# Kernel tuning notes

Hardware: AMD Instinct MI355X
Metric: run time of the kernel (lower is better)

The kernel has to match this reference:

```python
import jax, jax.numpy as jnp
import numpy as np

B, N, NUM_CLASS = 32, 4096, 40


def setup_inputs() -> dict:
    key = jax.random.key(0)
    ks = jax.random.split(key, 16)
    def w(k, o, i):
        return (jax.random.normal(k, (o, i), jnp.float32) / np.float32(np.sqrt(i)))
    inp = {"x": jax.random.uniform(ks[0], (B, N, 3), jnp.float32)}
    dims = [("sa1", 3, [64, 64, 128]), ("sa2", 3 + 128, [128, 128, 256]), ("sa3", 3 + 256, [256, 512, 1024])]
    ki = 1
    for name, cin, hs in dims:
        c = cin
        for j, h in enumerate(hs):
            inp[f"{name}_w{j}"] = w(jax.random.fold_in(ks[ki], j), h, c)
            inp[f"{name}_b{j}"] = jnp.zeros((h,), jnp.float32)
            c = h
        ki += 1
    for name, o, i in [("fc1", 512, 1024), ("fc2", 256, 512), ("fc3", NUM_CLASS, 256)]:
        inp[f"{name}_w"] = w(ks[ki], o, i)
        inp[f"{name}_b"] = jnp.zeros((o,), jnp.float32)
        ki += 1
    return inp


def _fps(xyz, npoint):
    # farthest point sampling for a single cloud, xyz: [N, 3] -> [npoint] indices
    n = xyz.shape[0]
    def body(carry, _):
        mind, last = carry
        d = jnp.sum((xyz - xyz[last]) ** 2, axis=-1)
        mind = jnp.minimum(mind, d)
        return (mind, jnp.argmax(mind).astype(jnp.int32)), last
    init = (jnp.full((n,), 1e10, xyz.dtype), jnp.int32(0))
    _, idx = jax.lax.scan(body, init, None, length=npoint)
    return idx


def _ball_query(new_xyz, xyz, radius, nsample):
    # new_xyz: [B,S,3], xyz: [B,N,3] -> [B,S,nsample] neighbor indices
    n = xyz.shape[1]
    sqd = (jnp.sum(new_xyz ** 2, -1)[:, :, None]
           + jnp.sum(xyz ** 2, -1)[:, None, :]
           - 2.0 * jnp.einsum('bsc,bnc->bsn', new_xyz, xyz))  # [B,S,N]
    gid = jnp.where(sqd <= radius ** 2, jnp.arange(n, dtype=jnp.int32), jnp.int32(n))
    gid = jnp.sort(gid, axis=-1)[..., :nsample]
    first = gid[..., :1]
    return jnp.where(gid == n, first, gid)


def _gather(x, idx):
    # x: [B,N,C], idx: [B,S,K] -> [B,S,K,C]
    return jax.vmap(lambda xb, ib: xb[ib])(x, idx)


def _shared_mlp(feat, layers):
    # feat: [..., C_in]; layers: list of (W [C_out,C_in], b [C_out]); 1x1 conv + ReLU (BN folded)
    for W, b in layers:
        feat = jax.nn.relu(jnp.einsum('bskc,oc->bsko', feat, W) + b)
    return feat


def _set_abstraction(xyz, feat, npoint, radius, nsample, layers):
    fidx = jax.vmap(lambda p: _fps(p, npoint))(xyz)            # [B,S]
    new_xyz = jax.vmap(lambda p, i: p[i])(xyz, fidx)           # [B,S,3]
    idx = _ball_query(new_xyz, xyz, radius, nsample)           # [B,S,K]
    gxyz = _gather(xyz, idx) - new_xyz[:, :, None, :]          # relative coords
    g = gxyz if feat is None else jnp.concatenate([gxyz, _gather(feat, idx)], axis=-1)
    g = _shared_mlp(g, layers)
    return new_xyz, jnp.max(g, axis=2)                         # max-pool over ball


def _sa_group_all(xyz, feat, layers):
    g = jnp.concatenate([xyz, feat], axis=-1)[:, None]         # [B,1,N,3+C]
    g = _shared_mlp(g, layers)
    return jnp.max(g, axis=2)[:, 0]                            # [B, 1024]


def reference(x,
              sa1_w0, sa1_b0, sa1_w1, sa1_b1, sa1_w2, sa1_b2,
              sa2_w0, sa2_b0, sa2_w1, sa2_b1, sa2_w2, sa2_b2,
              sa3_w0, sa3_b0, sa3_w1, sa3_b1, sa3_w2, sa3_b2,
              fc1_w, fc1_b, fc2_w, fc2_b, fc3_w, fc3_b):
    xyz, feat = x, None
    xyz, feat = _set_abstraction(xyz, feat, 512, 0.2, 32,
                                 [(sa1_w0, sa1_b0), (sa1_w1, sa1_b1), (sa1_w2, sa1_b2)])
    xyz, feat = _set_abstraction(xyz, feat, 128, 0.4, 64,
                                 [(sa2_w0, sa2_b0), (sa2_w1, sa2_b1), (sa2_w2, sa2_b2)])
    feat = _sa_group_all(xyz, feat,
                         [(sa3_w0, sa3_b0), (sa3_w1, sa3_b1), (sa3_w2, sa3_b2)])
    h = jax.nn.relu(feat @ fc1_w.T + fc1_b)
    h = jax.nn.relu(h @ fc2_w.T + fc2_b)
    logits = h @ fc3_w.T + fc3_b
    return jax.nn.softmax(logits, axis=-1)  # eval-mode output
```

## Files before the change

### kernel.cpp

```cpp
#include <hip/hip_runtime.h>
#include <math.h>

#define B_ 32
#define N_ 4096

typedef __attribute__((ext_vector_type(8))) short short8;
typedef __attribute__((ext_vector_type(4))) float f32x4;
typedef __attribute__((ext_vector_type(2))) float v2f;
typedef __attribute__((ext_vector_type(2))) unsigned u32x2;
typedef __attribute__((ext_vector_type(2))) unsigned long long u64x2;

__device__ __forceinline__ unsigned short f2bf(float f) {
    unsigned u = __float_as_uint(f);
    unsigned r = 0x7FFFu + ((u >> 16) & 1u);
    return (unsigned short)((u + r) >> 16);
}
__device__ __forceinline__ float bf2f(unsigned short h) {
    return __uint_as_float(((unsigned)h) << 16);
}
__device__ __forceinline__ void f2bfpair(float v, short& h, short& l) {
    unsigned short hh = f2bf(v);
    h = (short)hh;
    l = (short)f2bf(v - bf2f(hh));
}

#define KEY_BIAS 0x3F800000u

__device__ __forceinline__ double mk_key(unsigned hi, unsigned lo) {
    u32x2 p;
    p[0] = lo;
    p[1] = hi;
    return __builtin_bit_cast(double, p);
}

__device__ __forceinline__ unsigned long long u64max(unsigned long long a,
                                                     unsigned long long b) {
    return a > b ? a : b;
}
template<int CTRL>
__device__ __forceinline__ double dpp_dbl(double k) {
    unsigned long long u = (unsigned long long)__double_as_longlong(k);
    int lo = __builtin_amdgcn_mov_dpp((int)(unsigned)u, CTRL, 0xf, 0xf, true);
    int hi = __builtin_amdgcn_mov_dpp((int)(unsigned)(u >> 32), CTRL, 0xf, 0xf, true);
    unsigned long long r = ((unsigned long long)(unsigned)hi << 32) | (unsigned)lo;
    return __longlong_as_double((long long)r);
}
__device__ __forceinline__ double wave_argmax_dbl_leader(double key) {
    key = fmax(key, dpp_dbl<0x128>(key));
    key = fmax(key, dpp_dbl<0x124>(key));
    key = fmax(key, dpp_dbl<0x122>(key));
    key = fmax(key, dpp_dbl<0x121>(key));
    key = fmax(key, dpp_dbl<0x142>(key));
    key = fmax(key, dpp_dbl<0x143>(key));
    return key;
}

struct WDesc { const float* src; short* dh; short* dl; int R, C, Cp, blk0, perm; };
struct WDescs { WDesc d[8]; float* gfeat; int gblk0, gtotal; };

__device__ __forceinline__ void wprep_body(const WDescs& W, int blk, int tid) {
    if (blk >= W.gblk0) {
        const int i = (blk - W.gblk0) * 256 + tid;
        if (i < W.gtotal) W.gfeat[i] = 0.f;
        return;
    }
    int di = 0;
#pragma unroll
    for (int k = 1; k < 8; k++) di = (blk >= W.d[k].blk0) ? k : di;
    const WDesc D = W.d[di];
    const int i = (blk - D.blk0) * 256 + tid;
    if (i >= D.R * D.Cp) return;
    const int r = i / D.Cp, c = i % D.Cp;
    int cs;
    if (D.perm) cs = (c < 128) ? c + 3 : (c < 131 ? c - 128 : -1);
    else        cs = (c < D.C) ? c : -1;
    float v = (cs >= 0) ? D.src[r * D.C + cs] : 0.f;
    short h, l;
    f2bfpair(v, h, l);
    D.dh[i] = h; D.dl[i] = l;
}

template<int N, int NPOINT, int NT, int FPSB>
__global__ __launch_bounds__(NT, 1) void fps_wprep_kernel(
    const float* __restrict__ xyz, float* __restrict__ outXyz, WDescs W) {
#pragma clang fp contract(off)
    const int t = threadIdx.x;
    if (blockIdx.x >= FPSB) {
        wprep_body(W, blockIdx.x - FPSB, t);
        return;
    }
    const int b = blockIdx.x;
    constexpr int PPT = N / NT;
    constexpr int PP2 = PPT / 2;
    constexpr int NW = (NT + 63) / 64;
    __shared__ float ps[N][4];
    __shared__ __align__(16) double red[2][NW];
    __shared__ float outBuf[NPOINT * 3];
    const float* base = xyz + (size_t)b * N * 3;
    for (int j = t; j < N; j += NT) {
        ps[j][0] = base[j * 3 + 0];
        ps[j][1] = base[j * 3 + 1];
        ps[j][2] = base[j * 3 + 2];
    }
    __syncthreads();
    v2f px2[PP2], py2[PP2], pz2[PP2], mn2[PP2];
    unsigned nA[PP2], nB[PP2];
#pragma unroll
    for (int j = 0; j < PP2; j++) {
        const int p0 = t + (2 * j) * NT;
        const int p1 = t + (2 * j + 1) * NT;
        f32x4 a = *(const f32x4*)&ps[p0][0];
        f32x4 c = *(const f32x4*)&ps[p1][0];
        px2[j] = (v2f){a[0], c[0]};
        py2[j] = (v2f){a[1], c[1]};
        pz2[j] = (v2f){a[2], c[2]};
        mn2[j] = (v2f){1e10f, 1e10f};
        nA[j] = ~(unsigned)p0;
        nB[j] = ~(unsigned)p1;
    }
#pragma unroll
    for (int j = 0; j < PP2; j++)
        asm volatile("" : "+v"(px2[j]), "+v"(py2[j]), "+v"(pz2[j]));
    float lx = ps[0][0], ly = ps[0][1], lz = ps[0][2];
    if (t == 0) {
        outBuf[0] = lx; outBuf[1] = ly; outBuf[2] = lz;
    }
    for (int it = 1; it < NPOINT; it++) {
        const v2f lx2 = (v2f){lx, lx};
        const v2f ly2 = (v2f){ly, ly};
        const v2f lz2 = (v2f){lz, lz};
        double k0 = 0.0, k1 = 0.0, k2 = 0.0, k3 = 0.0;
#pragma unroll
        for (int j = 0; j < PP2; j++) {
            v2f dx = px2[j] - lx2;
            v2f dy = py2[j] - ly2;
            v2f dz = pz2[j] - lz2;
            v2f t0 = dx * dx, t1 = dy * dy, t2 = dz * dz;
            v2f d2 = (t0 + t1) + t2;
            v2f m = __builtin_elementwise_min(mn2[j], d2);
            mn2[j] = m;
            double da = mk_key(__float_as_uint(m[0]) + KEY_BIAS, nA[j]);
            double db = mk_key(__float_as_uint(m[1]) + KEY_BIAS, nB[j]);
            if (j & 1) { k2 = fmax(k2, da); k3 = fmax(k3, db); }
            else       { k0 = fmax(k0, da); k1 = fmax(k1, db); }
        }
        double key = fmax(fmax(k0, k1), fmax(k2, k3));
        key = wave_argmax_dbl_leader(key);
        const int par = it & 1;
        if ((t & 63) == 63) red[par][t >> 6] = key;
        __syncthreads();
        u64x2 r01 = *(const u64x2*)&red[par][0];
        u64x2 r23 = *(const u64x2*)&red[par][2];
        double b0 = __longlong_as_double((long long)r01[0]);
        double b1 = __longlong_as_double((long long)r01[1]);
        double b2 = __longlong_as_double((long long)r23[0]);
        double b3 = __longlong_as_double((long long)r23[1]);
        double best = fmax(fmax(b0, b1), fmax(b2, b3));
        const int fi = (int)(~(unsigned)(unsigned long long)__double_as_longlong(best));
        f32x4 c4 = *(const f32x4*)&ps[fi][0];
        lx = c4[0]; ly = c4[1]; lz = c4[2];
        if (t == 0) {
            outBuf[it * 3 + 0] = lx;
            outBuf[it * 3 + 1] = ly;
            outBuf[it * 3 + 2] = lz;
        }
    }
    __syncthreads();
    float* dst = outXyz + (size_t)b * NPOINT * 3;
    for (int j = t; j < NPOINT * 3; j += NT) dst[j] = outBuf[j];
}

template<int N, int NS>
__device__ __forceinline__ void ballquery_body(
    const float* __restrict__ xyz, const float* __restrict__ newXyz,
    int* __restrict__ outIdx, int S, float r2, int qid, int lane) {
#pragma clang fp contract(off)
    const int b = qid / S;
    const float* q = newXyz + (size_t)qid * 3;
    const float qx = q[0], qy = q[1], qz = q[2];
    const float qn = (qx * qx + qy * qy) + qz * qz;
    const float* base = xyz + (size_t)b * N * 3;
    int* dst = outIdx + (size_t)qid * NS;
    int cnt = 0, first = 0;
    for (int p0 = 0; p0 < N; p0 += 64) {
        const int p = p0 + lane;
        const float x = base[p * 3 + 0];
        const float y = base[p * 3 + 1];
        const float z = base[p * 3 + 2];
        const float pn = (x * x + y * y) + z * z;
        const float dot = (qx * x + qy * y) + qz * z;
        const float sqd = (qn + pn) - 2.0f * dot;
        const unsigned long long mask = __ballot(sqd <= r2);
        if (mask) {
            if (cnt == 0) first = p0 + __ffsll((unsigned long long)mask) - 1;
            const int prefix = __builtin_amdgcn_mbcnt_hi(
                (unsigned)(mask >> 32),
                __builtin_amdgcn_mbcnt_lo((unsigned)mask, 0));
            const bool in = (mask >> lane) & 1ull;
            const int pos = cnt + prefix;
            if (in && pos < NS) dst[pos] = p;
            cnt += __popcll(mask);
            if (cnt >= NS) break;
        }
    }
    for (int i = cnt + lane; i < NS; i += 64) dst[i] = first;
}

template<int FPB, int BQB, int NQ, int NS, int SQ, int NF, int NPF>
__global__ __launch_bounds__(256) void bq_fps_kernel(
    const float* __restrict__ xyzQ, const float* __restrict__ newXyzQ,
    int* __restrict__ outIdxQ, float r2,
    const float* __restrict__ xyzF, float* __restrict__ outXyzF) {
#pragma clang fp contract(off)
    const int t = threadIdx.x;
    const int lane = t & 63, wv = t >> 6;
    __shared__ float ps[NF][4];
    if (blockIdx.x >= FPB) {
        ballquery_body<NQ, NS>(xyzQ, newXyzQ, outIdxQ, SQ, r2,
                               (blockIdx.x - FPB) * 4 + wv, lane);
        return;
    }
    const int b = blockIdx.x;
    const float* base = xyzF + (size_t)b * NF * 3;
    for (int j = t; j < NF; j += 256) {
        ps[j][0] = base[j * 3 + 0];
        ps[j][1] = base[j * 3 + 1];
        ps[j][2] = base[j * 3 + 2];
    }
    __syncthreads();
    if (t >= 64) return;
    constexpr int PPT = NF / 64;
    constexpr int PP2 = PPT / 2;
    v2f px2[PP2], py2[PP2], pz2[PP2], mn2[PP2];
    unsigned nA[PP2], nB[PP2];
#pragma unroll
    for (int j = 0; j < PP2; j++) {
        const int p0 = t + (2 * j) * 64;
        const int p1 = t + (2 * j + 1) * 64;
        f32x4 a = *(const f32x4*)&ps[p0][0];
        f32x4 c = *(const f32x4*)&ps[p1][0];
        px2[j] = (v2f){a[0], c[0]};
        py2[j] = (v2f){a[1], c[1]};
        pz2[j] = (v2f){a[2], c[2]};
        mn2[j] = (v2f){1e10f, 1e10f};
        nA[j] = ~(unsigned)p0;
        nB[j] = ~(unsigned)p1;
    }
    float lx = ps[0][0], ly = ps[0][1], lz = ps[0][2];
    if (t == 0) {
        outXyzF[(size_t)b * NPF * 3 + 0] = lx;
        outXyzF[(size_t)b * NPF * 3 + 1] = ly;
        outXyzF[(size_t)b * NPF * 3 + 2] = lz;
    }
    for (int it = 1; it < NPF; it++) {
        const v2f lx2 = (v2f){lx, lx};
        const v2f ly2 = (v2f){ly, ly};
        const v2f lz2 = (v2f){lz, lz};
        double k0 = 0.0, k1 = 0.0;
#pragma unroll
        for (int j = 0; j < PP2; j++) {
            v2f dx = px2[j] - lx2;
            v2f dy = py2[j] - ly2;
            v2f dz = pz2[j] - lz2;
            v2f t0 = dx * dx, t1 = dy * dy, t2 = dz * dz;
            v2f d2 = (t0 + t1) + t2;
            v2f m = __builtin_elementwise_min(mn2[j], d2);
            mn2[j] = m;
            double da = mk_key(__float_as_uint(m[0]) + KEY_BIAS, nA[j]);
            double db = mk_key(__float_as_uint(m[1]) + KEY_BIAS, nB[j]);
            k0 = fmax(k0, da);
            k1 = fmax(k1, db);
        }
        double key = fmax(k0, k1);
        key = wave_argmax_dbl_leader(key);
        const int lo = __shfl(
            (int)(unsigned)(unsigned long long)__double_as_longlong(key), 63);
        const int fi = (int)(~(unsigned)lo);
        f32x4 c4 = *(const f32x4*)&ps[fi][0];
        lx = c4[0]; ly = c4[1]; lz = c4[2];
        if (t == 0) {
            outXyzF[((size_t)b * NPF + it) * 3 + 0] = lx;
            outXyzF[((size_t)b * NPF + it) * 3 + 1] = ly;
            outXyzF[((size_t)b * NPF + it) * 3 + 2] = lz;
        }
    }
}

template<int NT, int KS>
__device__ __forceinline__ void mfma_layer(
    const short* Aph, const short* Apl, const int sA,
    const short* __restrict__ Wph, const short* __restrict__ Wpl, const int sW,
    f32x4* acc, const int n0, const int mh, const int lr, const int lq) {
#pragma unroll
    for (int ks = 0; ks < KS; ks++) {
        const int ka = ks * 32 + lq * 8;
        short8 a_h[2], a_l[2];
#pragma unroll
        for (int mt = 0; mt < 2; mt++) {
            const int m = (mh * 2 + mt) * 16 + lr;
            a_h[mt] = *(const short8*)(Aph + m * sA + ka);
            a_l[mt] = *(const short8*)(Apl + m * sA + ka);
        }
#pragma unroll
        for (int nt = 0; nt < NT; nt++) {
            const int n = n0 + nt * 16 + lr;
            short8 b_h = *(const short8*)(Wph + (size_t)n * sW + ka);
            short8 b_l = *(const short8*)(Wpl + (size_t)n * sW + ka);
#pragma unroll
            for (int mt = 0; mt < 2; mt++) {
                f32x4 c = acc[mt * NT + nt];
                c = __builtin_amdgcn_mfma_f32_16x16x32_bf16(a_h[mt], b_h, c, 0, 0, 0);
                c = __builtin_amdgcn_mfma_f32_16x16x32_bf16(a_h[mt], b_l, c, 0, 0, 0);
                c = __builtin_amdgcn_mfma_f32_16x16x32_bf16(a_l[mt], b_h, c, 0, 0, 0);
                acc[mt * NT + nt] = c;
            }
        }
    }
}

template<int NT>
__device__ __forceinline__ void init_bias(f32x4* acc, const float* __restrict__ bias,
                                          const int n0, const int lr) {
#pragma unroll
    for (int nt = 0; nt < NT; nt++) {
        float bv = bias[n0 + nt * 16 + lr];
        f32x4 c = {bv, bv, bv, bv};
        acc[0 * NT + nt] = c;
        acc[1 * NT + nt] = c;
    }
}

template<int NT>
__device__ __forceinline__ void store_split(
    const f32x4* acc, short* Hp, short* Lp, const int stride,
    const int n0, const int mh, const int lr, const int lq) {
#pragma unroll
    for (int mt = 0; mt < 2; mt++)
#pragma unroll
        for (int nt = 0; nt < NT; nt++)
#pragma unroll
            for (int r = 0; r < 4; r++) {
                float v = fmaxf(acc[mt * NT + nt][r], 0.f);
                short h, l;
                f2bfpair(v, h, l);
                const int m = (mh * 2 + mt) * 16 + lq * 4 + r;
                const int n = n0 + nt * 16 + lr;
                Hp[m * stride + n] = h;
                Lp[m * stride + n] = l;
            }
}

#define T1 72
template<int BQ2B>
__global__ __launch_bounds__(256) void sa1_bq2_kernel(
    const float* __restrict__ x, const float* __restrict__ nxyz1,
    const int* __restrict__ idx,
    const float* __restrict__ w0, const float* __restrict__ b0,
    const short* __restrict__ w1h, const short* __restrict__ w1l,
    const float* __restrict__ b1,
    const short* __restrict__ w2h, const short* __restrict__ w2l,
    const float* __restrict__ b2,
    short* __restrict__ feat1h, short* __restrict__ feat1l,
    const float* __restrict__ nxyz2, int* __restrict__ idx2, float r2q) {
    const int t = threadIdx.x;
    const int lane = t & 63, wv = t >> 6;
    if (blockIdx.x < BQ2B) {
        ballquery_body<512, 64>(nxyz1, nxyz2, idx2, 128, r2q,
                                blockIdx.x * 4 + wv, lane);
        return;
    }
    const int g0 = (blockIdx.x - BQ2B) * 2;
    const int b = g0 >> 9;
    const int lr = lane & 15, lq = lane >> 4;
    const int mh = wv & 1, nh = wv >> 1;
    __shared__ float gx[64][4];
    __shared__ short H1h[64 * T1], H1l[64 * T1];
    __shared__ short H2h[64 * T1], H2l[64 * T1];
    if (t < 64) {
        int g = g0 + (t >> 5);
        int id = idx[(size_t)g * 32 + (t & 31)];
        const float* pp = x + ((size_t)b * N_ + id) * 3;
        const float* cc = nxyz1 + (size_t)g * 3;
        gx[t][0] = pp[0] - cc[0];
        gx[t][1] = pp[1] - cc[1];
        gx[t][2] = pp[2] - cc[2];
    }
    __syncthreads();
    {
        const int m = t >> 2, oc = (t & 3) * 16;
        float a0 = gx[m][0], a1 = gx[m][1], a2 = gx[m][2];
        short8 hv0, hv1, lv0, lv1;
#pragma unroll
        for (int i = 0; i < 16; i++) {
            int o = oc + i;
            float v = fmaf(w0[o * 3 + 0], a0,
                      fmaf(w0[o * 3 + 1], a1,
                      fmaf(w0[o * 3 + 2], a2, b0[o])));
            v = fmaxf(v, 0.f);
            short h, l;
            f2bfpair(v, h, l);
            if (i < 8) { hv0[i] = h; lv0[i] = l; }
            else       { hv1[i - 8] = h; lv1[i - 8] = l; }
        }
        *(short8*)&H1h[m * T1 + oc]     = hv0;
        *(short8*)&H1h[m * T1 + oc + 8] = hv1;
        *(short8*)&H1l[m * T1 + oc]     = lv0;
        *(short8*)&H1l[m * T1 + oc + 8] = lv1;
    }
    __syncthreads();
    {
        f32x4 acc[4];
        init_bias<2>(acc, b1, nh * 32, lr);
        mfma_layer<2, 2>(H1h, H1l, T1, w1h, w1l, 64, acc, nh * 32, mh, lr, lq);
        store_split<2>(acc, H2h, H2l, T1, nh * 32, mh, lr, lq);
    }
    __syncthreads();
    {
        f32x4 acc[8];
        init_bias<4>(acc, b2, nh * 64, lr);
        mfma_layer<4, 2>(H2h, H2l, T1, w2h, w2l, 64, acc, nh * 64, mh, lr, lq);
#pragma unroll
        for (int nt = 0; nt < 4; nt++) {
            float v = 0.f;
#pragma unroll
            for (int mt = 0; mt < 2; mt++)
#pragma unroll
                for (int r = 0; r < 4; r++)
                    v = fmaxf(v, acc[mt * 4 + nt][r]);
            v = fmaxf(v, __shfl_xor(v, 16));
            v = fmaxf(v, __shfl_xor(v, 32));
            if (lane < 16) {
                short h, l;
                f2bfpair(v, h, l);
                size_t o = (size_t)(g0 + mh) * 128 + nh * 64 + nt * 16 + lane;
                feat1h[o] = h;
                feat1l[o] = l;
            }
        }
    }
}

#define S1 168
#define S2 136
__global__ __launch_bounds__(256) void sa2_mfma_kernel(
    const float* __restrict__ xyz1,
    const short* __restrict__ feat1h, const short* __restrict__ feat1l,
    const float* __restrict__ newXyz, const int* __restrict__ idx,
    const short* __restrict__ w0h, const short* __restrict__ w0l,
    const float* __restrict__ b0,
    const short* __restrict__ w1h, const short* __restrict__ w1l,
    const float* __restrict__ b1,
    const short* __restrict__ w2h, const short* __restrict__ w2l,
    const float* __restrict__ b2,
    short* __restrict__ a3h, short* __restrict__ a3l) {
    const int g = blockIdx.x;
    const int b = g >> 7;
    const int t = threadIdx.x;
    const int lane = t & 63, wv = t >> 6;
    const int lr = lane & 15, lq = lane >> 4;
    const int mh = wv & 1, nh = wv >> 1;
    __shared__ short Ah[64 * S1], Al[64 * S1];
    __shared__ short Hh[64 * S2], Hl[64 * S2];
    __shared__ float pmax[2][256];
    __shared__ int ids[64];
    if (t < 64) ids[t] = idx[(size_t)g * 64 + t];
    __syncthreads();
    {
        const int m = t >> 2, q = t & 3;
        const int id = ids[m];
        const size_t frow = ((size_t)b * 512 + id) * 128;
#pragma unroll
        for (int c8 = 0; c8 < 4; c8++) {
            const int k = q * 32 + c8 * 8;
            *(short8*)&Ah[m * S1 + k] = *(const short8*)(feat1h + frow + k);
            *(short8*)&Al[m * S1 + k] = *(const short8*)(feat1l + frow + k);
        }
        if (t < 64) {
            const int id2 = ids[t];
            short8 zz = {0, 0, 0, 0, 0, 0, 0, 0};
            *(short8*)&Ah[t * S1 + 128] = zz;
            *(short8*)&Ah[t * S1 + 136] = zz;
            *(short8*)&Ah[t * S1 + 144] = zz;
            *(short8*)&Ah[t * S1 + 152] = zz;
            *(short8*)&Al[t * S1 + 128] = zz;
            *(short8*)&Al[t * S1 + 136] = zz;
            *(short8*)&Al[t * S1 + 144] = zz;
            *(short8*)&Al[t * S1 + 152] = zz;
            const float* prow = xyz1 + ((size_t)b * 512 + id2) * 3;
            const float* crow = newXyz + (size_t)g * 3;
#pragma unroll
            for (int c = 0; c < 3; c++) {
                short h, l;
                f2bfpair(prow[c] - crow[c], h, l);
                Ah[t * S1 + 128 + c] = h;
                Al[t * S1 + 128 + c] = l;
            }
        }
    }
    __syncthreads();
    {
        f32x4 acc[8];
        init_bias<4>(acc, b0, nh * 64, lr);
        mfma_layer<4, 5>(Ah, Al, S1, w0h, w0l, 160, acc, nh * 64, mh, lr, lq);
        store_split<4>(acc, Hh, Hl, S2, nh * 64, mh, lr, lq);
    }
    __syncthreads();
    {
        f32x4 acc[8];
        init_bias<4>(acc, b1, nh * 64, lr);
        mfma_layer<4, 4>(Hh, Hl, S2, w1h, w1l, 128, acc, nh * 64, mh, lr, lq);
        store_split<4>(acc, Ah, Al, S2, nh * 64, mh, lr, lq);
    }
    __syncthreads();
    {
        f32x4 acc[16];
        init_bias<8>(acc, b2, nh * 128, lr);
        mfma_layer<8, 4>(Ah, Al, S2, w2h, w2l, 128, acc, nh * 128, mh, lr, lq);
#pragma unroll
        for (int nt = 0; nt < 8; nt++) {
            float v = 0.f;
#pragma unroll
            for (int mt = 0; mt < 2; mt++)
#pragma unroll
                for (int r = 0; r < 4; r++)
                    v = fmaxf(v, acc[mt * 8 + nt][r]);
            v = fmaxf(v, __shfl_xor(v, 16));
            v = fmaxf(v, __shfl_xor(v, 32));
            if (lane < 16) pmax[mh][nh * 128 + nt * 16 + lane] = v;
        }
    }
    __syncthreads();
    {
        float v = fmaxf(pmax[0][t], pmax[1][t]);
        short h, l;
        f2bfpair(v, h, l);
        a3h[(size_t)g * 288 + 3 + t] = h;
        a3l[(size_t)g * 288 + 3 + t] = l;
        if (t < 3) {
            f2bfpair(newXyz[(size_t)g * 3 + t], h, l);
            a3h[(size_t)g * 288 + t] = h;
            a3l[(size_t)g * 288 + t] = l;
        }
        if (t >= 227) {
            a3h[(size_t)g * 288 + t + 32] = 0;
            a3l[(size_t)g * 288 + t + 32] = 0;
        }
    }
}

template<int OUT_MODE>
__global__ __launch_bounds__(256) void mfma_gemm_kernel(
    const short* __restrict__ Agh, const short* __restrict__ Agl, const int Kp,
    const short* __restrict__ Wh, const short* __restrict__ Wl,
    const float* __restrict__ bias,
    float* __restrict__ outF, short* __restrict__ outH,
    short* __restrict__ outL, const int N) {
    const int t = threadIdx.x;
    const int lane = t & 63, wv = t >> 6;
    const int lr = lane & 15, lq = lane >> 4;
    const int mh = wv & 1, nh = wv >> 1;
    const int m0 = blockIdx.y * 64;
    const int n0 = blockIdx.x * 128 + nh * 64;
    __shared__ short Ah[64 * 40], Al[64 * 40];
    f32x4 acc[8];
#pragma unroll
    for (int nt = 0; nt < 4; nt++) {
        float bv = bias[n0 + nt * 16 + lr];
        f32x4 c = {bv, bv, bv, bv};
        acc[nt] = c; acc[4 + nt] = c;
    }
    const int srow = t >> 2, sk = (t & 3) * 8;
    for (int kt = 0; kt < Kp; kt += 32) {
        {
            const size_t src = (size_t)(m0 + srow) * Kp + kt + sk;
            *(short8*)&Ah[srow * 40 + sk] = *(const short8*)(Agh + src);
            *(short8*)&Al[srow * 40 + sk] = *(const short8*)(Agl + src);
        }
        __syncthreads();
        short8 a_h[2], a_l[2];
#pragma unroll
        for (int mt = 0; mt < 2; mt++) {
            const int m = mh * 32 + mt * 16 + lr;
            a_h[mt] = *(const short8*)&Ah[m * 40 + lq * 8];
            a_l[mt] = *(const short8*)&Al[m * 40 + lq * 8];
        }
#pragma unroll
        for (int nt = 0; nt < 4; nt++) {
            const int n = n0 + nt * 16 + lr;
            short8 b_h = *(const short8*)(Wh + (size_t)n * Kp + kt + lq * 8);
            short8 b_l = *(const short8*)(Wl + (size_t)n * Kp + kt + lq * 8);
#pragma unroll
            for (int mt = 0; mt < 2; mt++) {
                f32x4 c = acc[mt * 4 + nt];
                c = __builtin_amdgcn_mfma_f32_16x16x32_bf16(a_h[mt], b_h, c, 0, 0, 0);
                c = __builtin_amdgcn_mfma_f32_16x16x32_bf16(a_h[mt], b_l, c, 0, 0, 0);
                c = __builtin_amdgcn_mfma_f32_16x16x32_bf16(a_l[mt], b_h, c, 0, 0, 0);
                acc[mt * 4 + nt] = c;
            }
        }
        __syncthreads();
    }
    if (OUT_MODE == 2) {
        const int batch = blockIdx.y >> 1;
#pragma unroll
        for (int nt = 0; nt < 4; nt++) {
            float v = 0.f;
#pragma unroll
            for (int mt = 0; mt < 2; mt++)
#pragma unroll
                for (int r = 0; r < 4; r++)
                    v = fmaxf(v, acc[mt * 4 + nt][r]);
            v = fmaxf(v, __shfl_xor(v, 16));
            v = fmaxf(v, __shfl_xor(v, 32));
            if (lane < 16)
                atomicMax((int*)&outF[(size_t)batch * N + n0 + nt * 16 + lane],
                          __float_as_int(v));
        }
        return;
    }
#pragma unroll
    for (int mt = 0; mt < 2; mt++)
#pragma unroll
        for (int nt = 0; nt < 4; nt++)
#pragma unroll
            for (int r = 0; r < 4; r++) {
                const int m = m0 + mh * 32 + mt * 16 + lq * 4 + r;
                const int n = n0 + nt * 16 + lr;
                float v = fmaxf(acc[mt * 4 + nt][r], 0.f);
                short h, l;
                f2bfpair(v, h, l);
                outH[(size_t)m * N + n] = h;
                outL[(size_t)m * N + n] = l;
            }
}

template<int K, int OPW, int ACT>
__global__ __launch_bounds__(256) void fc_kernel(
    const float* __restrict__ in, const float* __restrict__ w,
    const float* __restrict__ bias, float* __restrict__ out, const int O) {
    const int batch = blockIdx.y;
    const int t = threadIdx.x, lane = t & 63, wv = t >> 6;
    __shared__ float f[K];
    for (int j = t; j < K; j += 256) f[j] = in[batch * K + j];
    __syncthreads();
    const int o0 = blockIdx.x * (4 * OPW) + wv * OPW;
#pragma unroll
    for (int i = 0; i < OPW; i++) {
        const int o = o0 + i;
        const float* wr = w + (size_t)o * K;
        float a = 0.f;
#pragma unroll
        for (int c = lane; c < K; c += 64) a = fmaf(wr[c], f[c], a);
#pragma unroll
        for (int off = 32; off > 0; off >>= 1) a += __shfl_xor(a, off);
        if (lane == 0) {
            float v = a + bias[o];
            out[batch * O + o] = ACT ? fmaxf(v, 0.f) : v;
        }
    }
}

__global__ __launch_bounds__(256) void fc3_softmax_kernel(
    const float* __restrict__ in, const float* __restrict__ w3,
    const float* __restrict__ b3, float* __restrict__ out) {
    const int b = blockIdx.x, t = threadIdx.x, lane = t & 63, wv = t >> 6;
    __shared__ float f[256];
    __shared__ float lg[40];
    f[t] = in[b * 256 + t];
    __syncthreads();
#pragma unroll
    for (int i = 0; i < 10; i++) {
        const int o = wv * 10 + i;
        const float* wr = w3 + (size_t)o * 256;
        float a = 0.f;
#pragma unroll
        for (int c = lane; c < 256; c += 64) a = fmaf(wr[c], f[c], a);
#pragma unroll
        for (int off = 32; off > 0; off >>= 1) a += __shfl_xor(a, off);
        if (lane == 0) lg[o] = a + b3[o];
    }
    __syncthreads();
    if (t < 64) {
        float v = (t < 40) ? lg[t] : -INFINITY;
        float m = v;
#pragma unroll
        for (int off = 32; off > 0; off >>= 1) m = fmaxf(m, __shfl_xor(m, off));
        float e = (t < 40) ? expf(v - m) : 0.f;
        float s = e;
#pragma unroll
        for (int off = 32; off > 0; off >>= 1) s += __shfl_xor(s, off);
        if (t < 40) out[b * 40 + t] = e / s;
    }
}

extern "C" void kernel_launch(void* const* d_in, const int* in_sizes, int n_in,
                              void* d_out, int out_size, void* d_ws, size_t ws_size,
                              hipStream_t stream) {
    (void)in_sizes; (void)n_in; (void)out_size; (void)ws_size;
    const float* x      = (const float*)d_in[0];
    const float* sa1w0  = (const float*)d_in[1];
    const float* sa1b0  = (const float*)d_in[2];
    const float* sa1w1  = (const float*)d_in[3];
    const float* sa1b1  = (const float*)d_in[4];
    const float* sa1w2  = (const float*)d_in[5];
    const float* sa1b2  = (const float*)d_in[6];
    const float* sa2w0  = (const float*)d_in[7];
    const float* sa2b0  = (const float*)d_in[8];
    const float* sa2w1  = (const float*)d_in[9];
    const float* sa2b1  = (const float*)d_in[10];
    const float* sa2w2  = (const float*)d_in[11];
    const float* sa2b2  = (const float*)d_in[12];
    const float* sa3w0  = (const float*)d_in[13];
    const float* sa3b0  = (const float*)d_in[14];
    const float* sa3w1  = (const float*)d_in[15];
    const float* sa3b1  = (const float*)d_in[16];
    const float* sa3w2  = (const float*)d_in[17];
    const float* sa3b2  = (const float*)d_in[18];
    const float* fc1w   = (const float*)d_in[19];
    const float* fc1b   = (const float*)d_in[20];
    const float* fc2w   = (const float*)d_in[21];
    const float* fc2b   = (const float*)d_in[22];
    const float* fc3w   = (const float*)d_in[23];
    const float* fc3b   = (const float*)d_in[24];
    float* outp = (float*)d_out;

    char* ws = (char*)d_ws;
    size_t off = 0;
    auto alloc = [&](size_t bytes) {
        void* p = ws + off;
        off += (bytes + 255) & ~(size_t)255;
        return p;
    };
    float* nxyz1   = (float*)alloc((size_t)B_ * 512 * 3 * 4);
    int*   idx1    = (int*)  alloc((size_t)B_ * 512 * 32 * 4);
    short* feat1h  = (short*)alloc((size_t)B_ * 512 * 128 * 2);
    short* feat1l  = (short*)alloc((size_t)B_ * 512 * 128 * 2);
    float* nxyz2   = (float*)alloc((size_t)B_ * 128 * 3 * 4);
    int*   idx2    = (int*)  alloc((size_t)B_ * 128 * 64 * 4);
    short* a3h     = (short*)alloc((size_t)4096 * 288 * 2);
    short* a3l     = (short*)alloc((size_t)4096 * 288 * 2);
    short* h3ah    = (short*)alloc((size_t)4096 * 256 * 2);
    short* h3al    = (short*)alloc((size_t)4096 * 256 * 2);
    short* h3bh    = (short*)alloc((size_t)4096 * 512 * 2);
    short* h3bl    = (short*)alloc((size_t)4096 * 512 * 2);
    float* gfeat   = (float*)alloc((size_t)B_ * 1024 * 4);
    float* h1      = (float*)alloc((size_t)B_ * 512 * 4);
    float* h2      = (float*)alloc((size_t)B_ * 256 * 4);
    short* w1h_s1 = (short*)alloc((size_t)64 * 64 * 2);
    short* w1l_s1 = (short*)alloc((size_t)64 * 64 * 2);
    short* w2h_s1 = (short*)alloc((size_t)128 * 64 * 2);
    short* w2l_s1 = (short*)alloc((size_t)128 * 64 * 2);
    short* w0h_s2 = (short*)alloc((size_t)128 * 160 * 2);
    short* w0l_s2 = (short*)alloc((size_t)128 * 160 * 2);
    short* w1h_s2 = (short*)alloc((size_t)128 * 128 * 2);
    short* w1l_s2 = (short*)alloc((size_t)128 * 128 * 2);
    short* w2h_s2 = (short*)alloc((size_t)256 * 128 * 2);
    short* w2l_s2 = (short*)alloc((size_t)256 * 128 * 2);
    short* w0h_s3 = (short*)alloc((size_t)256 * 288 * 2);
    short* w0l_s3 = (short*)alloc((size_t)256 * 288 * 2);
    short* w1h_s3 = (short*)alloc((size_t)512 * 256 * 2);
    short* w1l_s3 = (short*)alloc((size_t)512 * 256 * 2);
    short* w2h_s3 = (short*)alloc((size_t)1024 * 512 * 2);
    short* w2l_s3 = (short*)alloc((size_t)1024 * 512 * 2);

    {
        WDescs W;
        const float* srcs[8] = {sa1w1, sa1w2, sa2w0, sa2w1, sa2w2, sa3w0, sa3w1, sa3w2};
        short* dhs[8] = {w1h_s1, w2h_s1, w0h_s2, w1h_s2, w2h_s2, w0h_s3, w1h_s3, w2h_s3};
        short* dls[8] = {w1l_s1, w2l_s1, w0l_s2, w1l_s2, w2l_s2, w0l_s3, w1l_s3, w2l_s3};
        int Rs[8]  = {64, 128, 128, 128, 256, 256, 512, 1024};
        int Cs[8]  = {64, 64, 131, 128, 128, 259, 256, 512};
        int Cps[8] = {64, 64, 160, 128, 128, 288, 256, 512};
        int blk = 0;
        for (int k = 0; k < 8; k++) {
            W.d[k] = {srcs[k], dhs[k], dls[k], Rs[k], Cs[k], Cps[k], blk,
                      (k == 2) ? 1 : 0};
            blk += (Rs[k] * Cps[k] + 255) / 256;
        }
        W.gfeat = gfeat;
        W.gblk0 = blk;
        W.gtotal = B_ * 1024;
        blk += (B_ * 1024 + 255) / 256;
        fps_wprep_kernel<4096, 512, 256, B_><<<B_ + blk, 256, 0, stream>>>(
            x, nxyz1, W);
    }

    bq_fps_kernel<B_, 4096, 4096, 32, 512, 512, 128>
        <<<B_ + 4096, 256, 0, stream>>>(
            x, nxyz1, idx1, 0.04f, nxyz1, nxyz2);
    sa1_bq2_kernel<1024><<<1024 + 8192, 256, 0, stream>>>(
        x, nxyz1, idx1, sa1w0, sa1b0,
        w1h_s1, w1l_s1, sa1b1, w2h_s1, w2l_s1, sa1b2, feat1h, feat1l,
        nxyz2, idx2, 0.16f);
    sa2_mfma_kernel<<<B_ * 128, 256, 0, stream>>>(
        nxyz1, feat1h, feat1l, nxyz2, idx2,
        w0h_s2, w0l_s2, sa2b0, w1h_s2, w1l_s2, sa2b1, w2h_s2, w2l_s2, sa2b2,
        a3h, a3l);
    mfma_gemm_kernel<1><<<dim3(2, 64), 256, 0, stream>>>(
        a3h, a3l, 288, w0h_s3, w0l_s3, sa3b0, nullptr, h3ah, h3al, 256);
    mfma_gemm_kernel<1><<<dim3(4, 64), 256, 0, stream>>>(
        h3ah, h3al, 256, w1h_s3, w1l_s3, sa3b1, nullptr, h3bh, h3bl, 512);
    mfma_gemm_kernel<2><<<dim3(8, 64), 256, 0, stream>>>(
        h3bh, h3bl, 512, w2h_s3, w2l_s3, sa3b2, gfeat, nullptr, nullptr, 1024);
    fc_kernel<1024, 16, 1><<<dim3(8, B_), 256, 0, stream>>>(
        gfeat, fc1w, fc1b, h1, 512);
    fc_kernel<512, 16, 1><<<dim3(4, B_), 256, 0, stream>>>(
        h1, fc2w, fc2b, h2, 256);
    fc3_softmax_kernel<<<B_, 256, 0, stream>>>(h2, fc3w, fc3b, outp);
}
```

Measured before the change: 930.7 us.

## Stream FPS centroids to persistent ball-query workers via flagged global mailboxes

Before, the first-level ball query waited for the whole farthest point sampling kernel to finish. Now FPS blocks publish each new centroid to a per-point mailbox (xy packed together, z plus a sequence number stored with release), and 736 persistent worker blocks spin on those flags and run the ball query for each centroid as soon as it appears. Weight prep runs in the same workers. The second-level FPS moves into the SA1 MLP kernel through a shared-memory arena, and the second ball query becomes its own small kernel. The goal is to hide ball-query and prep latency behind the serial FPS loop, at the cost of spin-wait traffic, dependence on all FPS blocks being co-resident with the workers, and a memset of the mailboxes.

```diff
diff --git a/kernel.cpp b/kernel.cpp
--- a/kernel.cpp
+++ b/kernel.cpp
@@ -31,11 +31,6 @@
     p[0] = lo;
     p[1] = hi;
     return __builtin_bit_cast(double, p);
-}
-
-__device__ __forceinline__ unsigned long long u64max(unsigned long long a,
-                                                     unsigned long long b) {
-    return a > b ? a : b;
 }
 template<int CTRL>
 __device__ __forceinline__ double dpp_dbl(double k) {
@@ -53,6 +48,15 @@
     key = fmax(key, dpp_dbl<0x142>(key));
     key = fmax(key, dpp_dbl<0x143>(key));
     return key;
+}
+
+struct __align__(16) QPub { unsigned long long xy, zs; };
+
+__device__ __forceinline__ unsigned long long pk2(float a, float b) {
+    return ((unsigned long long)__float_as_uint(b) << 32) | __float_as_uint(a);
+}
+__device__ __forceinline__ unsigned long long pkzs(float z, unsigned seq) {
+    return ((unsigned long long)seq << 32) | __float_as_uint(z);
 }
 
 struct WDesc { const float* src; short* dh; short* dl; int R, C, Cp, blk0, perm; };
@@ -80,107 +84,12 @@
     D.dh[i] = h; D.dl[i] = l;
 }
 
-template<int N, int NPOINT, int NT, int FPSB>
-__global__ __launch_bounds__(NT, 1) void fps_wprep_kernel(
-    const float* __restrict__ xyz, float* __restrict__ outXyz, WDescs W) {
+template<int N, int NS>
+__device__ __forceinline__ void ballquery_scan(
+    const float* __restrict__ base, float qx, float qy, float qz,
+    int* __restrict__ dst, float r2, int lane) {
 #pragma clang fp contract(off)
-    const int t = threadIdx.x;
-    if (blockIdx.x >= FPSB) {
-        wprep_body(W, blockIdx.x - FPSB, t);
-        return;
-    }
-    const int b = blockIdx.x;
-    constexpr int PPT = N / NT;
-    constexpr int PP2 = PPT / 2;
-    constexpr int NW = (NT + 63) / 64;
-    __shared__ float ps[N][4];
-    __shared__ __align__(16) double red[2][NW];
-    __shared__ float outBuf[NPOINT * 3];
-    const float* base = xyz + (size_t)b * N * 3;
-    for (int j = t; j < N; j += NT) {
-        ps[j][0] = base[j * 3 + 0];
-        ps[j][1] = base[j * 3 + 1];
-        ps[j][2] = base[j * 3 + 2];
-    }
-    __syncthreads();
-    v2f px2[PP2], py2[PP2], pz2[PP2], mn2[PP2];
-    unsigned nA[PP2], nB[PP2];
-#pragma unroll
-    for (int j = 0; j < PP2; j++) {
-        const int p0 = t + (2 * j) * NT;
-        const int p1 = t + (2 * j + 1) * NT;
-        f32x4 a = *(const f32x4*)&ps[p0][0];
-        f32x4 c = *(const f32x4*)&ps[p1][0];
-        px2[j] = (v2f){a[0], c[0]};
-        py2[j] = (v2f){a[1], c[1]};
-        pz2[j] = (v2f){a[2], c[2]};
-        mn2[j] = (v2f){1e10f, 1e10f};
-        nA[j] = ~(unsigned)p0;
-        nB[j] = ~(unsigned)p1;
-    }
-#pragma unroll
-    for (int j = 0; j < PP2; j++)
-        asm volatile("" : "+v"(px2[j]), "+v"(py2[j]), "+v"(pz2[j]));
-    float lx = ps[0][0], ly = ps[0][1], lz = ps[0][2];
-    if (t == 0) {
-        outBuf[0] = lx; outBuf[1] = ly; outBuf[2] = lz;
-    }
-    for (int it = 1; it < NPOINT; it++) {
-        const v2f lx2 = (v2f){lx, lx};
-        const v2f ly2 = (v2f){ly, ly};
-        const v2f lz2 = (v2f){lz, lz};
-        double k0 = 0.0, k1 = 0.0, k2 = 0.0, k3 = 0.0;
-#pragma unroll
-        for (int j = 0; j < PP2; j++) {
-            v2f dx = px2[j] - lx2;
-            v2f dy = py2[j] - ly2;
-            v2f dz = pz2[j] - lz2;
-            v2f t0 = dx * dx, t1 = dy * dy, t2 = dz * dz;
-            v2f d2 = (t0 + t1) + t2;
-            v2f m = __builtin_elementwise_min(mn2[j], d2);
-            mn2[j] = m;
-            double da = mk_key(__float_as_uint(m[0]) + KEY_BIAS, nA[j]);
-            double db = mk_key(__float_as_uint(m[1]) + KEY_BIAS, nB[j]);
-            if (j & 1) { k2 = fmax(k2, da); k3 = fmax(k3, db); }
-            else       { k0 = fmax(k0, da); k1 = fmax(k1, db); }
-        }
-        double key = fmax(fmax(k0, k1), fmax(k2, k3));
-        key = wave_argmax_dbl_leader(key);
-        const int par = it & 1;
-        if ((t & 63) == 63) red[par][t >> 6] = key;
-        __syncthreads();
-        u64x2 r01 = *(const u64x2*)&red[par][0];
-        u64x2 r23 = *(const u64x2*)&red[par][2];
-        double b0 = __longlong_as_double((long long)r01[0]);
-        double b1 = __longlong_as_double((long long)r01[1]);
-        double b2 = __longlong_as_double((long long)r23[0]);
-        double b3 = __longlong_as_double((long long)r23[1]);
-        double best = fmax(fmax(b0, b1), fmax(b2, b3));
-        const int fi = (int)(~(unsigned)(unsigned long long)__double_as_longlong(best));
-        f32x4 c4 = *(const f32x4*)&ps[fi][0];
-        lx = c4[0]; ly = c4[1]; lz = c4[2];
-        if (t == 0) {
-            outBuf[it * 3 + 0] = lx;
-            outBuf[it * 3 + 1] = ly;
-            outBuf[it * 3 + 2] = lz;
-        }
-    }
-    __syncthreads();
-    float* dst = outXyz + (size_t)b * NPOINT * 3;
-    for (int j = t; j < NPOINT * 3; j += NT) dst[j] = outBuf[j];
-}
-
-template<int N, int NS>
-__device__ __forceinline__ void ballquery_body(
-    const float* __restrict__ xyz, const float* __restrict__ newXyz,
-    int* __restrict__ outIdx, int S, float r2, int qid, int lane) {
-#pragma clang fp contract(off)
-    const int b = qid / S;
-    const float* q = newXyz + (size_t)qid * 3;
-    const float qx = q[0], qy = q[1], qz = q[2];
     const float qn = (qx * qx + qy * qy) + qz * qz;
-    const float* base = xyz + (size_t)b * N * 3;
-    int* dst = outIdx + (size_t)qid * NS;
     int cnt = 0, first = 0;
     for (int p0 = 0; p0 < N; p0 += 64) {
         const int p = p0 + lane;
@@ -206,57 +115,93 @@
     for (int i = cnt + lane; i < NS; i += 64) dst[i] = first;
 }
 
-template<int FPB, int BQB, int NQ, int NS, int SQ, int NF, int NPF>
-__global__ __launch_bounds__(256) void bq_fps_kernel(
-    const float* __restrict__ xyzQ, const float* __restrict__ newXyzQ,
-    int* __restrict__ outIdxQ, float r2,
-    const float* __restrict__ xyzF, float* __restrict__ outXyzF) {
+template<int N, int NS>
+__device__ __forceinline__ void ballquery_body(
+    const float* __restrict__ xyz, const float* __restrict__ newXyz,
+    int* __restrict__ outIdx, int S, float r2, int qid, int lane) {
+    const int b = qid / S;
+    const float* q = newXyz + (size_t)qid * 3;
+    ballquery_scan<N, NS>(xyz + (size_t)b * N * 3, q[0], q[1], q[2],
+                          outIdx + (size_t)qid * NS, r2, lane);
+}
+
+template<int N, int NPOINT, int NT, int FPSB, int WBLK>
+__global__ __launch_bounds__(NT, 3) void fps_bq1_kernel(
+    const float* __restrict__ xyz, float* __restrict__ outXyz,
+    int* __restrict__ outIdx1, float r2q, QPub* __restrict__ qpub,
+    WDescs W, int witems) {
 #pragma clang fp contract(off)
     const int t = threadIdx.x;
     const int lane = t & 63, wv = t >> 6;
-    __shared__ float ps[NF][4];
-    if (blockIdx.x >= FPB) {
-        ballquery_body<NQ, NS>(xyzQ, newXyzQ, outIdxQ, SQ, r2,
-                               (blockIdx.x - FPB) * 4 + wv, lane);
+    if (blockIdx.x >= FPSB) {
+        const int wb = blockIdx.x - FPSB;
+        for (int item = wb; item < witems; item += WBLK)
+            wprep_body(W, item, t);
+        const int wgid = (wb << 2) | wv;
+        for (int q = wgid; q < B_ * NPOINT; q += WBLK * 4) {
+            const int g = q & (NPOINT - 1);
+            QPub* qp = qpub + q;
+            while ((unsigned)(__hip_atomic_load(&qp->zs, __ATOMIC_RELAXED,
+                                                __HIP_MEMORY_SCOPE_AGENT) >> 32)
+                   != (unsigned)(g + 1))
+                __builtin_amdgcn_s_sleep(2);
+            const unsigned long long wzs = __hip_atomic_load(
+                &qp->zs, __ATOMIC_ACQUIRE, __HIP_MEMORY_SCOPE_AGENT);
+            const unsigned long long wxy = __hip_atomic_load(
+                &qp->xy, __ATOMIC_RELAXED, __HIP_MEMORY_SCOPE_AGENT);
+            const float qx = __uint_as_float((unsigned)wxy);
+            const float qy = __uint_as_float((unsigned)(wxy >> 32));
+            const float qz = __uint_as_float((unsigned)wzs);
+            ballquery_scan<N, 32>(xyz + (size_t)(q / NPOINT) * N * 3,
+                                  qx, qy, qz,
+                                  outIdx1 + (size_t)q * 32, r2q, lane);
+        }
         return;
     }
+    __builtin_amdgcn_s_setprio(1);
     const int b = blockIdx.x;
-    const float* base = xyzF + (size_t)b * NF * 3;
-    for (int j = t; j < NF; j += 256) {
+    constexpr int PPT = N / NT;
+    constexpr int PP2 = PPT / 2;
+    constexpr int NW = (NT + 63) / 64;
+    __shared__ float ps[N][3];
+    __shared__ __align__(16) double red[2][NW];
+    const float* base = xyz + (size_t)b * N * 3;
+    for (int j = t; j < N; j += NT) {
         ps[j][0] = base[j * 3 + 0];
         ps[j][1] = base[j * 3 + 1];
         ps[j][2] = base[j * 3 + 2];
     }
     __syncthreads();
-    if (t >= 64) return;
-    constexpr int PPT = NF / 64;
-    constexpr int PP2 = PPT / 2;
     v2f px2[PP2], py2[PP2], pz2[PP2], mn2[PP2];
     unsigned nA[PP2], nB[PP2];
 #pragma unroll
     for (int j = 0; j < PP2; j++) {
-        const int p0 = t + (2 * j) * 64;
-        const int p1 = t + (2 * j + 1) * 64;
-        f32x4 a = *(const f32x4*)&ps[p0][0];
-        f32x4 c = *(const f32x4*)&ps[p1][0];
-        px2[j] = (v2f){a[0], c[0]};
-        py2[j] = (v2f){a[1], c[1]};
-        pz2[j] = (v2f){a[2], c[2]};
+        const int p0 = t + (2 * j) * NT;
+        const int p1 = t + (2 * j + 1) * NT;
+        px2[j] = (v2f){ps[p0][0], ps[p1][0]};
+        py2[j] = (v2f){ps[p0][1], ps[p1][1]};
+        pz2[j] = (v2f){ps[p0][2], ps[p1][2]};
         mn2[j] = (v2f){1e10f, 1e10f};
         nA[j] = ~(unsigned)p0;
         nB[j] = ~(unsigned)p1;
     }
+#pragma unroll
+    for (int j = 0; j < PP2; j++)
+        asm volatile("" : "+v"(px2[j]), "+v"(py2[j]), "+v"(pz2[j]));
     float lx = ps[0][0], ly = ps[0][1], lz = ps[0][2];
+    QPub* qp = qpub + (size_t)b * NPOINT;
+    float* outB = outXyz + (size_t)b * NPOINT * 3;
+    float pz_prev = lz;
     if (t == 0) {
-        outXyzF[(size_t)b * NPF * 3 + 0] = lx;
-        outXyzF[(size_t)b * NPF * 3 + 1] = ly;
-        outXyzF[(size_t)b * NPF * 3 + 2] = lz;
-    }
-    for (int it = 1; it < NPF; it++) {
+        outB[0] = lx; outB[1] = ly; outB[2] = lz;
+        __hip_atomic_store(&qp[0].xy, pk2(lx, ly), __ATOMIC_RELAXED,
+                           __HIP_MEMORY_SCOPE_AGENT);
+    }
+    for (int it = 1; it < NPOINT; it++) {
         const v2f lx2 = (v2f){lx, lx};
         const v2f ly2 = (v2f){ly, ly};
         const v2f lz2 = (v2f){lz, lz};
-        double k0 = 0.0, k1 = 0.0;
+        double k0 = 0.0, k1 = 0.0, k2 = 0.0, k3 = 0.0;
 #pragma unroll
         for (int j = 0; j < PP2; j++) {
             v2f dx = px2[j] - lx2;
@@ -268,22 +213,37 @@
             mn2[j] = m;
             double da = mk_key(__float_as_uint(m[0]) + KEY_BIAS, nA[j]);
             double db = mk_key(__float_as_uint(m[1]) + KEY_BIAS, nB[j]);
-            k0 = fmax(k0, da);
-            k1 = fmax(k1, db);
-        }
-        double key = fmax(k0, k1);
+            if (j & 1) { k2 = fmax(k2, da); k3 = fmax(k3, db); }
+            else       { k0 = fmax(k0, da); k1 = fmax(k1, db); }
+        }
+        double key = fmax(fmax(k0, k1), fmax(k2, k3));
         key = wave_argmax_dbl_leader(key);
-        const int lo = __shfl(
-            (int)(unsigned)(unsigned long long)__double_as_longlong(key), 63);
-        const int fi = (int)(~(unsigned)lo);
-        f32x4 c4 = *(const f32x4*)&ps[fi][0];
-        lx = c4[0]; ly = c4[1]; lz = c4[2];
+        const int par = it & 1;
+        if ((t & 63) == 63) red[par][t >> 6] = key;
+        __syncthreads();
+        u64x2 r01 = *(const u64x2*)&red[par][0];
+        u64x2 r23 = *(const u64x2*)&red[par][2];
+        double b0 = __longlong_as_double((long long)r01[0]);
+        double b1 = __longlong_as_double((long long)r01[1]);
+        double b2 = __longlong_as_double((long long)r23[0]);
+        double b3 = __longlong_as_double((long long)r23[1]);
+        double best = fmax(fmax(b0, b1), fmax(b2, b3));
+        const int fi = (int)(~(unsigned)(unsigned long long)__double_as_longlong(best));
+        lx = ps[fi][0]; ly = ps[fi][1]; lz = ps[fi][2];
         if (t == 0) {
-            outXyzF[((size_t)b * NPF + it) * 3 + 0] = lx;
-            outXyzF[((size_t)b * NPF + it) * 3 + 1] = ly;
-            outXyzF[((size_t)b * NPF + it) * 3 + 2] = lz;
-        }
-    }
+            __hip_atomic_store(&qp[it - 1].zs, pkzs(pz_prev, (unsigned)it),
+                               __ATOMIC_RELEASE, __HIP_MEMORY_SCOPE_AGENT);
+            __hip_atomic_store(&qp[it].xy, pk2(lx, ly), __ATOMIC_RELAXED,
+                               __HIP_MEMORY_SCOPE_AGENT);
+            pz_prev = lz;
+            outB[it * 3 + 0] = lx;
+            outB[it * 3 + 1] = ly;
+            outB[it * 3 + 2] = lz;
+        }
+    }
+    if (t == 0)
+        __hip_atomic_store(&qp[NPOINT - 1].zs, pkzs(pz_prev, (unsigned)NPOINT),
+                           __ATOMIC_RELEASE, __HIP_MEMORY_SCOPE_AGENT);
 }
 
 template<int NT, int KS>
@@ -351,8 +311,9 @@
 }
 
 #define T1 72
-template<int BQ2B>
-__global__ __launch_bounds__(256) void sa1_bq2_kernel(
+#define ARENA_BYTES 37888
+template<int FPB, int NF, int NPF>
+__global__ __launch_bounds__(256) void fps2_sa1_kernel(
     const float* __restrict__ x, const float* __restrict__ nxyz1,
     const int* __restrict__ idx,
     const float* __restrict__ w0, const float* __restrict__ b0,
@@ -361,21 +322,89 @@
     const short* __restrict__ w2h, const short* __restrict__ w2l,
     const float* __restrict__ b2,
     short* __restrict__ feat1h, short* __restrict__ feat1l,
-    const float* __restrict__ nxyz2, int* __restrict__ idx2, float r2q) {
+    float* __restrict__ outXyzF) {
     const int t = threadIdx.x;
     const int lane = t & 63, wv = t >> 6;
-    if (blockIdx.x < BQ2B) {
-        ballquery_body<512, 64>(nxyz1, nxyz2, idx2, 128, r2q,
-                                blockIdx.x * 4 + wv, lane);
+    __shared__ __align__(16) char arena[ARENA_BYTES];
+    if (blockIdx.x < FPB) {
+#pragma clang fp contract(off)
+        __builtin_amdgcn_s_setprio(1);
+        float (*ps)[4] = (float(*)[4])arena;
+        const int b = blockIdx.x;
+        const float* base = nxyz1 + (size_t)b * NF * 3;
+        for (int j = t; j < NF; j += 256) {
+            ps[j][0] = base[j * 3 + 0];
+            ps[j][1] = base[j * 3 + 1];
+            ps[j][2] = base[j * 3 + 2];
+        }
+        __syncthreads();
+        if (t >= 64) return;
+        constexpr int PPT = NF / 64;
+        constexpr int PP2 = PPT / 2;
+        v2f px2[PP2], py2[PP2], pz2[PP2], mn2[PP2];
+        unsigned nA[PP2], nB[PP2];
+#pragma unroll
+        for (int j = 0; j < PP2; j++) {
+            const int p0 = t + (2 * j) * 64;
+            const int p1 = t + (2 * j + 1) * 64;
+            f32x4 a = *(const f32x4*)&ps[p0][0];
+            f32x4 c = *(const f32x4*)&ps[p1][0];
+            px2[j] = (v2f){a[0], c[0]};
+            py2[j] = (v2f){a[1], c[1]};
+            pz2[j] = (v2f){a[2], c[2]};
+            mn2[j] = (v2f){1e10f, 1e10f};
+            nA[j] = ~(unsigned)p0;
+            nB[j] = ~(unsigned)p1;
+        }
+        float lx = ps[0][0], ly = ps[0][1], lz = ps[0][2];
+        if (t == 0) {
+            outXyzF[(size_t)b * NPF * 3 + 0] = lx;
+            outXyzF[(size_t)b * NPF * 3 + 1] = ly;
+            outXyzF[(size_t)b * NPF * 3 + 2] = lz;
+        }
+        for (int it = 1; it < NPF; it++) {
+            const v2f lx2 = (v2f){lx, lx};
+            const v2f ly2 = (v2f){ly, ly};
+            const v2f lz2 = (v2f){lz, lz};
+            double k0 = 0.0, k1 = 0.0;
+#pragma unroll
+            for (int j = 0; j < PP2; j++) {
+                v2f dx = px2[j] - lx2;
+                v2f dy = py2[j] - ly2;
+                v2f dz = pz2[j] - lz2;
+                v2f t0 = dx * dx, t1 = dy * dy, t2 = dz * dz;
+                v2f d2 = (t0 + t1) + t2;
+                v2f m = __builtin_elementwise_min(mn2[j], d2);
+                mn2[j] = m;
+                double da = mk_key(__float_as_uint(m[0]) + KEY_BIAS, nA[j]);
+                double db = mk_key(__float_as_uint(m[1]) + KEY_BIAS, nB[j]);
+                k0 = fmax(k0, da);
+                k1 = fmax(k1, db);
+            }
+            double key = fmax(k0, k1);
+            key = wave_argmax_dbl_leader(key);
+            const int lo = __shfl(
+                (int)(unsigned)(unsigned long long)__double_as_longlong(key), 63);
+            const int fi = (int)(~(unsigned)lo);
+            f32x4 c4 = *(const f32x4*)&ps[fi][0];
+            lx = c4[0]; ly = c4[1]; lz = c4[2];
+            if (t == 0) {
+                outXyzF[((size_t)b * NPF + it) * 3 + 0] = lx;
+                outXyzF[((size_t)b * NPF + it) * 3 + 1] = ly;
+                outXyzF[((size_t)b * NPF + it) * 3 + 2] = lz;
+            }
+        }
         return;
     }
-    const int g0 = (blockIdx.x - BQ2B) * 2;
+    const int g0 = (blockIdx.x - FPB) * 2;
     const int b = g0 >> 9;
     const int lr = lane & 15, lq = lane >> 4;
     const int mh = wv & 1, nh = wv >> 1;
-    __shared__ float gx[64][4];
-    __shared__ short H1h[64 * T1], H1l[64 * T1];
-    __shared__ short H2h[64 * T1], H2l[64 * T1];
+    float (*gx)[4] = (float(*)[4])arena;
+    short* H1h = (short*)(arena + 1024);
+    short* H1l = (short*)(arena + 10240);
+    short* H2h = (short*)(arena + 19456);
+    short* H2l = (short*)(arena + 28672);
     if (t < 64) {
         int g = g0 + (t >> 5);
         int id = idx[(size_t)g * 32 + (t & 31)];
@@ -438,6 +467,14 @@
             }
         }
     }
+}
+
+__global__ __launch_bounds__(256) void bq2_kernel(
+    const float* __restrict__ nxyz1, const float* __restrict__ nxyz2,
+    int* __restrict__ idx2, float r2q) {
+    const int t = threadIdx.x, lane = t & 63, wv = t >> 6;
+    ballquery_body<512, 64>(nxyz1, nxyz2, idx2, 128, r2q,
+                            blockIdx.x * 4 + wv, lane);
 }
 
 #define S1 168
@@ -732,6 +769,7 @@
         return p;
     };
     float* nxyz1   = (float*)alloc((size_t)B_ * 512 * 3 * 4);
+    QPub*  qpub    = (QPub*) alloc((size_t)B_ * 512 * sizeof(QPub));
     int*   idx1    = (int*)  alloc((size_t)B_ * 512 * 32 * 4);
     short* feat1h  = (short*)alloc((size_t)B_ * 512 * 128 * 2);
     short* feat1l  = (short*)alloc((size_t)B_ * 512 * 128 * 2);
@@ -763,6 +801,8 @@
     short* w2h_s3 = (short*)alloc((size_t)1024 * 512 * 2);
     short* w2l_s3 = (short*)alloc((size_t)1024 * 512 * 2);
 
+    hipMemsetAsync(qpub, 0, (size_t)B_ * 512 * sizeof(QPub), stream);
+
     {
         WDescs W;
         const float* srcs[8] = {sa1w1, sa1w2, sa2w0, sa2w1, sa2w2, sa3w0, sa3w1, sa3w2};
@@ -780,18 +820,17 @@
         W.gfeat = gfeat;
         W.gblk0 = blk;
         W.gtotal = B_ * 1024;
-        blk += (B_ * 1024 + 255) / 256;
-        fps_wprep_kernel<4096, 512, 256, B_><<<B_ + blk, 256, 0, stream>>>(
-            x, nxyz1, W);
-    }
-
-    bq_fps_kernel<B_, 4096, 4096, 32, 512, 512, 128>
-        <<<B_ + 4096, 256, 0, stream>>>(
-            x, nxyz1, idx1, 0.04f, nxyz1, nxyz2);
-    sa1_bq2_kernel<1024><<<1024 + 8192, 256, 0, stream>>>(
+        int witems = blk + (B_ * 1024 + 255) / 256;
+        fps_bq1_kernel<4096, 512, 256, B_, 736>
+            <<<B_ + 736, 256, 0, stream>>>(
+                x, nxyz1, idx1, 0.04f, qpub, W, witems);
+    }
+
+    fps2_sa1_kernel<B_, 512, 128><<<B_ + 8192, 256, 0, stream>>>(
         x, nxyz1, idx1, sa1w0, sa1b0,
         w1h_s1, w1l_s1, sa1b1, w2h_s1, w2l_s1, sa1b2, feat1h, feat1l,
-        nxyz2, idx2, 0.16f);
+        nxyz2);
+    bq2_kernel<<<1024, 256, 0, stream>>>(nxyz1, nxyz2, idx2, 0.16f);
     sa2_mfma_kernel<<<B_ * 128, 256, 0, stream>>>(
         nxyz1, feat1h, feat1l, nxyz2, idx2,
         w0h_s2, w0l_s2, sa2b0, w1h_s2, w1l_s2, sa2b1, w2h_s2, w2l_s2, sa2b2,
```

Result: slower. 1.229 ms (+32.0%).
